# Kernel optimization log

Measured on AMD Instinct MI355X. Metric: run time of the kernel, lower is better.

## Reference

```python
import jax, jax.numpy as jnp
import numpy as np
from jax import lax

EPS = 1e-8
SLOPE = 0.2

def _modconv(x, wv, W, b, sW, sB, demodulate, pad):
    # StyleGAN2 modulated conv, expressed in the equivalent fused form:
    # scale input by per-sample style s, shared-weight conv, then demodulate output.
    s = wv @ sW.T + sB                                   # [B, Cin]
    y = lax.conv_general_dilated(
        x * s[:, :, None, None], W, (1, 1), [(pad, pad), (pad, pad)],
        dimension_numbers=("NCHW", "OIHW", "NCHW"))      # [B, Cout, H, W]
    if demodulate:
        # d[b,o] = 1/sqrt(sum_{i,k,k} (W[o,i,k,k]*s[b,i])^2 + eps)
        d = lax.rsqrt(jnp.einsum("oihw,bi->bo", W * W, s * s) + EPS)
        y = y * d[:, :, None, None]
    return y + b[None, :, None, None]

def _up2(x):
    B, C, H, W = x.shape
    # matches torch F.interpolate(scale_factor=2, mode='bilinear', align_corners=False)
    return jax.image.resize(x, (B, C, 2 * H, 2 * W), method="bilinear")

def setup_inputs() -> dict:
    B, CIN, COUT, NZ, H = 8, 512, 512, 512, 32
    key = jax.random.key(0)
    ks = jax.random.split(key, 20)
    wscale3 = 1.0 / np.sqrt(CIN * 9)   # kaiming-ish equalized-lr scale baked into weights
    wscale1 = 1.0 / np.sqrt(COUT)
    sscale = 1.0 / np.sqrt(NZ)
    return {
        "maps": jax.random.normal(ks[0], (B, CIN, H, H), jnp.float32),
        "w": jax.random.normal(ks[1], (B, NZ), jnp.float32),
        "rgb": jax.random.normal(ks[2], (B, 3, H, H), jnp.float32),
        "noise0": jax.random.normal(ks[3], (B, 1, 2 * H, 2 * H), jnp.float32),
        "noise1": jax.random.normal(ks[4], (B, 1, 2 * H, 2 * H), jnp.float32),
        "w0": jax.random.normal(ks[5], (COUT, CIN, 3, 3), jnp.float32) * wscale3,
        "b0": jnp.zeros((COUT,), jnp.float32),
        "sW0": jax.random.normal(ks[6], (CIN, NZ), jnp.float32) * sscale,
        "sB0": jnp.ones((CIN,), jnp.float32),
        "ns0": jax.random.normal(ks[7], (COUT,), jnp.float32) * 0.1,
        "w1": jax.random.normal(ks[8], (COUT, COUT, 3, 3), jnp.float32) * wscale3,
        "b1": jnp.zeros((COUT,), jnp.float32),
        "sW1": jax.random.normal(ks[9], (COUT, NZ), jnp.float32) * sscale,
        "sB1": jnp.ones((COUT,), jnp.float32),
        "ns1": jax.random.normal(ks[10], (COUT,), jnp.float32) * 0.1,
        "rgbW": jax.random.normal(ks[11], (3, COUT, 1, 1), jnp.float32) * wscale1,
        "rgbB": jnp.zeros((3,), jnp.float32),
        "rgbSW": jax.random.normal(ks[12], (COUT, NZ), jnp.float32) * sscale,
        "rgbSB": jnp.ones((COUT,), jnp.float32),
    }

def reference(maps, w, rgb, noise0, noise1,
              w0, b0, sW0, sB0, ns0,
              w1, b1, sW1, sB1, ns1,
              rgbW, rgbB, rgbSW, rgbSB):
    rgb = _up2(rgb)
    x = _up2(maps)
    # layer 0: modulated conv 3x3 + noise + leakyrelu
    x = _modconv(x, w, w0, b0, sW0, sB0, True, 1)
    x = x + ns0[None, :, None, None] * noise0
    x = jnp.where(x >= 0, x, SLOPE * x)
    # layer 1
    x = _modconv(x, w, w1, b1, sW1, sB1, True, 1)
    x = x + ns1[None, :, None, None] * noise1
    x = jnp.where(x >= 0, x, SLOPE * x)
    # to_rgb: modulated 1x1 conv, no demodulation
    rgb_out = rgb + _modconv(x, w, rgbW, rgbB, rgbSW, rgbSB, False, 0)
    return (rgb_out, x)
```

## Files before the change

kernel.cpp:

```cpp
#include <hip/hip_runtime.h>

typedef unsigned short u16;
typedef short bf16x8 __attribute__((ext_vector_type(8)));
typedef float f32x4 __attribute__((ext_vector_type(4)));
typedef u16 u16x4 __attribute__((ext_vector_type(4)));
typedef u16 u16x8 __attribute__((ext_vector_type(8)));
typedef unsigned u32x4 __attribute__((ext_vector_type(4)));

__device__ __forceinline__ float b2f(u16 v) {
  union { unsigned u; float f; } x; x.u = ((unsigned)v) << 16; return x.f;
}
__device__ __forceinline__ u16 f2b(float f) {
  unsigned u = __float_as_uint(f);
  unsigned r = (u + 0x7FFFu + ((u >> 16) & 1u)) >> 16;
  return (u16)r;
}
__device__ __forceinline__ float rin(const void* p, size_t i, int bf) {
  return bf ? b2f(((const u16*)p)[i]) : ((const float*)p)[i];
}
__device__ __forceinline__ void async16(const void* g, void* l) {
  __builtin_amdgcn_global_load_lds((const __attribute__((address_space(1))) unsigned*)g,
                                   (__attribute__((address_space(3))) unsigned*)l, 16, 0, 0);
}
__device__ __forceinline__ int detect_bf(const unsigned* __restrict__ w0raw, int tid, int* shflag) {
  if (tid < 64) {
    const unsigned lo = w0raw[tid] & 0xFFFFu;
    const unsigned e = (lo >> 7) & 0xFFu;
    const unsigned long long bad = __ballot(e < 100u || e > 126u);
    if (tid == 0) *shflag = (bad == 0ull) ? 1 : 0;
  }
  __syncthreads();
  return *shflag;
}

__global__ void styleall_kernel(const void* __restrict__ w,
                                const void* __restrict__ sW0, const void* __restrict__ sB0,
                                const void* __restrict__ sW1, const void* __restrict__ sB1,
                                const void* __restrict__ sWR, const void* __restrict__ sBR,
                                float* __restrict__ s0, float* __restrict__ s1,
                                float* __restrict__ sR, const unsigned* __restrict__ w0raw) {
  __shared__ int shflag;
  const int tid = threadIdx.x;
  const int bf = detect_bf(w0raw, tid, &shflag);
  const int mat = blockIdx.z, b = blockIdx.y, oc = blockIdx.x;
  const void* sW = (mat == 0) ? sW0 : ((mat == 1) ? sW1 : sWR);
  const void* sB = (mat == 0) ? sB0 : ((mat == 1) ? sB1 : sBR);
  float* out = (mat == 0) ? s0 : ((mat == 1) ? s1 : sR);
  const int i = oc * 64 + (tid >> 2), q = tid & 3;
  float acc = 0.f;
  if (bf) {
    const u16* rp = (const u16*)sW + (size_t)i * 512 + q * 128;
    const u16* wp = (const u16*)w + b * 512 + q * 128;
    for (int z = 0; z < 128; z += 8) {
      u16x8 a = *(const u16x8*)(rp + z), c = *(const u16x8*)(wp + z);
#pragma unroll
      for (int j = 0; j < 8; ++j) acc += b2f(a[j]) * b2f(c[j]);
    }
  } else {
    const float* rp = (const float*)sW + (size_t)i * 512 + q * 128;
    const float* wp = (const float*)w + b * 512 + q * 128;
    for (int z = 0; z < 128; z += 4) {
      f32x4 a = *(const f32x4*)(rp + z), c = *(const f32x4*)(wp + z);
#pragma unroll
      for (int j = 0; j < 4; ++j) acc += a[j] * c[j];
    }
  }
  acc += __shfl_xor(acc, 1, 64);
  acc += __shfl_xor(acc, 2, 64);
  if (q == 0) out[b * 512 + i] = acc + rin(sB, i, bf);
}

__global__ void demod_kernel(const void* __restrict__ W0, const void* __restrict__ W1,
                             const float* __restrict__ s0, const float* __restrict__ s1,
                             float* __restrict__ dm0, float* __restrict__ dm1,
                             u16* __restrict__ Wp0, u16* __restrict__ Wp1,
                             const unsigned* __restrict__ w0raw) {
  __shared__ int shflag;
  __shared__ float wl[4608];
  __shared__ float wsq[512];
  const int tid = threadIdx.x, lane = tid & 63, wv = tid >> 6;
  const int bf = detect_bf(w0raw, tid, &shflag);
  const int o = blockIdx.x, layer = blockIdx.y;
  const void* W = layer ? W1 : W0;
  const float* s = layer ? s1 : s0;
  float* d = layer ? dm1 : dm0;
  u16* Wp = layer ? Wp1 : Wp0;

  if (bf) {
    const u16* src = (const u16*)W + (size_t)o * 4608;
    for (int e = tid; e < 576; e += 256) {
      u16x8 v = *(const u16x8*)(src + e * 8);
#pragma unroll
      for (int j = 0; j < 8; ++j) wl[e * 8 + j] = b2f(v[j]);
    }
  } else {
    const float* src = (const float*)W + (size_t)o * 4608;
    for (int e = tid; e < 1152; e += 256) {
      f32x4 v = *(const f32x4*)(src + e * 4);
#pragma unroll
      for (int j = 0; j < 4; ++j) wl[e * 4 + j] = v[j];
    }
  }
  __syncthreads();
  for (int i = tid; i < 512; i += 256) {
    float ss = 0.f;
#pragma unroll
    for (int t = 0; t < 9; ++t) {
      const float f = wl[i * 9 + t];
      ss += f * f;
      Wp[t * 262144 + o * 512 + i] = f2b(f);
    }
    wsq[i] = ss;
  }
  __syncthreads();
#pragma unroll
  for (int bb = 0; bb < 2; ++bb) {
    const int b = wv * 2 + bb;
    float part = 0.f;
    for (int i = lane; i < 512; i += 64) { const float sv = s[b * 512 + i]; part += wsq[i] * sv * sv; }
#pragma unroll
    for (int st = 1; st < 64; st <<= 1) part += __shfl_xor(part, st, 64);
    if (lane == 0) d[b * 512 + o] = rsqrtf(part + 1e-8f);
  }
}

__global__ void prep_kernel(u16* __restrict__ actB, u32x4* __restrict__ zr, int NB) {
  const int id = blockIdx.x, tid = threadIdx.x;
  if (id < NB * 65) {
    const int bl = id / 65, sub = id - bl * 65;
    const int c = sub * 256 + tid;
    const int px = c >> 6, seg = c & 63;
    int oy, ox;
    if (px < 66)       { oy = 0;  ox = px; }
    else if (px < 132) { oy = 65; ox = px - 66; }
    else { const int e = px - 132; oy = 1 + (e >> 1); ox = (e & 1) * 65; }
    u32x4 z = {0, 0, 0, 0};
    *(u32x4*)&actB[((size_t)(bl * 4356) + oy * 66 + ox) * 512 + seg * 8] = z;
  } else {
    const int c = (id - NB * 65) * 256 + tid;
    if (c < 24832) { u32x4 z = {0, 0, 0, 0}; zr[c] = z; }
  }
}

__global__ void upsample_kernel(const void* __restrict__ maps, const float* __restrict__ s,
                                void* __restrict__ outb, int b_base,
                                const unsigned* __restrict__ w0raw) {
  __shared__ int shflag;
  __shared__ float it[32][2][33];
  const int tid = threadIdx.x;
  const int bf = detect_bf(w0raw, tid, &shflag);
  const size_t esz = bf ? 2 : 4;
  u16* xg = (u16*)((char*)outb + (98304 + (size_t)(b_base >> 2) * 8388608) * esz);
  int oy, i0, bl;
  if (gridDim.z == 8) {
    const int id = blockIdx.x + (blockIdx.y << 6) + (blockIdx.z << 10);
    bl = id & 7; const int r = id >> 3; oy = r & 63; i0 = (r >> 6) << 5;
  } else {
    oy = blockIdx.x; i0 = blockIdx.y << 5; bl = blockIdx.z;
  }
  const int bg = b_base + bl;
  const int m = oy >> 1;
  int iy0, iy1; float wy0, wy1;
  if ((oy & 1) == 0) { iy0 = (m > 0) ? m - 1 : 0; iy1 = m; wy0 = 0.25f; wy1 = 0.75f; }
  else               { iy0 = m; iy1 = (m < 31) ? m + 1 : 31; wy0 = 0.75f; wy1 = 0.25f; }
#pragma unroll
  for (int k = 0; k < 8; ++k) {
    const int e = tid + k * 256;
    const int c = e >> 6, wsel = (e >> 5) & 1, x = e & 31;
    const int iy = wsel ? iy1 : iy0;
    it[c][wsel][x] = rin(maps, ((size_t)(bg * 512 + i0 + c) * 32 + iy) * 32 + x, bf);
  }
  __syncthreads();
#pragma unroll
  for (int k = 0; k < 8; ++k) {
    const int e = tid + k * 256;
    const int xx = e >> 5, c = e & 31;
    const int mx = xx >> 1;
    int ix0, ix1; float wx0, wx1;
    if ((xx & 1) == 0) { ix0 = (mx > 0) ? mx - 1 : 0; ix1 = mx; wx0 = 0.25f; wx1 = 0.75f; }
    else               { ix0 = mx; ix1 = (mx < 31) ? mx + 1 : 31; wx0 = 0.75f; wx1 = 0.25f; }
    const float r0 = wx0 * it[c][0][ix0] + wx1 * it[c][0][ix1];
    const float r1 = wx0 * it[c][1][ix0] + wx1 * it[c][1][ix1];
    const float v = (wy0 * r0 + wy1 * r1) * s[bg * 512 + i0 + c];
    xg[((size_t)(bl * 4096) + oy * 64 + xx) * 512 + i0 + c] = f2b(v);
  }
}

template <int L>
__global__ __launch_bounds__(256, 2) void conv_kernel(
    void* __restrict__ outb, u16* __restrict__ actBp,
    const u16* __restrict__ Wp, const float* __restrict__ dmod,
    const void* __restrict__ bias, const void* __restrict__ nsc,
    const void* __restrict__ noise, const float* __restrict__ saux,
    const u16* __restrict__ zbuf, const void* __restrict__ rgbW,
    float* __restrict__ rgbacc, int b_base,
    const unsigned* __restrict__ w0raw) {
  __shared__ __attribute__((aligned(16))) u16 lds[32768];
  __shared__ float rgbWl[L == 1 ? 1536 : 4];
  __shared__ int shflag;
  const int tid = threadIdx.x, lane = tid & 63, w = tid >> 6;
  const int bf = detect_bf(w0raw, tid, &shflag);
  const size_t esz = bf ? 2 : 4;

  const int lin = blockIdx.x + (blockIdx.y << 5) + (blockIdx.z << 7);
  const int cpx = (int)(gridDim.z << 4);
  const int wg = (lin & 7) * cpx + (lin >> 3);
  const int bl = wg >> 7, rem = wg & 127;
  const int o0 = (rem >> 5) << 7, n0 = (rem & 31) << 7;
  const int bg = b_base + bl;
  const int wm = w >> 1, wn = w & 1;

  if constexpr (L == 1) {
    for (int e = tid; e < 1536; e += 256) rgbWl[e] = rin(rgbW, e, bf);
  }
  const u16* xg = (const u16*)((const char*)outb +
                  (98304 + (size_t)(b_base >> 2) * 8388608) * esz);

  const int q = lane >> 4, m15 = lane & 15;
  const int lro = m15 * 64 + ((q ^ (lane & 7)) * 8);
  const int srow8 = lane >> 3, schunk = (lane & 7) ^ srow8;
  const size_t aAst = (size_t)(o0 + srow8) * 512 + schunk * 8;

  const int sbase = (w & 1) * 2 + (w >> 1) * 8;
  int oyv[4], oxv[4];
  size_t pB[4];
  {
    const int kk4[4] = {sbase, sbase + 1, sbase + 4, sbase + 5};
#pragma unroll
    for (int j = 0; j < 4; ++j) {
      const int p = n0 + kk4[j] * 8 + srow8;
      const int oy = p >> 6, ox = p & 63;
      oyv[j] = oy; oxv[j] = ox;
      pB[j] = ((size_t)bl * 4356 + oy * 66 + ox) * 512 + schunk * 8;
    }
  }

  const u16* bBase[4];
  int koff, aoffu;
  auto setTap = [&](int tn_) {
    const int ty_ = (tn_ * 11) >> 5, tx_ = tn_ - ty_ * 3;
    koff = 0;
    aoffu = tn_ * 262144;
    if constexpr (L == 0) {
#pragma unroll
      for (int j = 0; j < 4; ++j) {
        const int iy_ = oyv[j] + ty_ - 1, ix_ = oxv[j] + tx_ - 1;
        bBase[j] = (((unsigned)iy_ < 64u) & ((unsigned)ix_ < 64u))
          ? (xg + ((size_t)((bl << 12) + (iy_ << 6) + ix_) * 512 + schunk * 8))
          : (zbuf + schunk * 8);
      }
    } else {
      const int sb_ = (ty_ * 66 + tx_) * 512;
#pragma unroll
      for (int j = 0; j < 4; ++j) bBase[j] = actBp + pB[j] + sb_;
    }
  };

#define STAGE_A(k_) \
  async16(Wp + aAst + (size_t)aoffu + (size_t)(k_) * 4096, &lds[stb + (k_) * 512])
#define STAGE_B(j_, k_) \
  async16(bBase[j_] + koff, &lds[stb + 8192 + (k_) * 512])

  f32x4 acc[4][4] = {};
  {
    setTap(0);
    const int stb = 0;
    STAGE_A(sbase); STAGE_A(sbase + 1);
    STAGE_A(sbase + 4); STAGE_A(sbase + 5);
    STAGE_B(0, sbase); STAGE_B(1, sbase + 1);
    STAGE_B(2, sbase + 4); STAGE_B(3, sbase + 5);
  }
  koff = 64; aoffu = 64;
  asm volatile("s_waitcnt vmcnt(0)" ::: "memory");
  __builtin_amdgcn_s_barrier();

  int arA  = wm * 4096 + lro;
  int arAx = wm * 4096 + (lro ^ 32);
  int arB  = 8192 + wn * 4096 + lro;
  int arBx = 8192 + wn * 4096 + (lro ^ 32);
  int stb  = 16384;

  bf16x8 afr[2][2], bfr[4][2];
#pragma unroll 1
  for (int s = 0; s < 72; ++s) {
    const int s1 = s + 1, ok = (s1 < 72);
    if (ok && (s1 & 7) == 0) setTap(s1 >> 3);

#pragma unroll
    for (int ni = 0; ni < 4; ++ni) {
      bfr[ni][0] = *(const bf16x8*)&lds[arB + ni * 1024];
      bfr[ni][1] = *(const bf16x8*)&lds[arBx + ni * 1024];
    }
#pragma unroll
    for (int mi = 0; mi < 2; ++mi) {
      afr[mi][0] = *(const bf16x8*)&lds[arA + mi * 1024];
      afr[mi][1] = *(const bf16x8*)&lds[arAx + mi * 1024];
    }
    if (ok) {
      STAGE_A(sbase); STAGE_A(sbase + 1);
      STAGE_B(0, sbase); STAGE_B(1, sbase + 1);
    }
    __builtin_amdgcn_s_setprio(1);
#pragma unroll
    for (int mi = 0; mi < 2; ++mi)
#pragma unroll
      for (int ni = 0; ni < 4; ++ni)
#pragma unroll
        for (int kk = 0; kk < 2; ++kk)
          acc[mi][ni] = __builtin_amdgcn_mfma_f32_16x16x32_bf16(
              afr[mi][kk], bfr[ni][kk], acc[mi][ni], 0, 0, 0);
    __builtin_amdgcn_s_setprio(0);
    if (ok) { asm volatile("s_waitcnt vmcnt(4)" ::: "memory"); }
    else    { asm volatile("s_waitcnt vmcnt(0)" ::: "memory"); }
    __builtin_amdgcn_s_barrier();

#pragma unroll
    for (int mi = 0; mi < 2; ++mi) {
      afr[mi][0] = *(const bf16x8*)&lds[arA + 2048 + mi * 1024];
      afr[mi][1] = *(const bf16x8*)&lds[arAx + 2048 + mi * 1024];
    }
    if (ok) {
      STAGE_B(2, sbase + 4); STAGE_B(3, sbase + 5);
      STAGE_A(sbase + 4); STAGE_A(sbase + 5);
    }
    __builtin_amdgcn_s_setprio(1);
#pragma unroll
    for (int mi = 0; mi < 2; ++mi)
#pragma unroll
      for (int ni = 0; ni < 4; ++ni)
#pragma unroll
        for (int kk = 0; kk < 2; ++kk)
          acc[2 + mi][ni] = __builtin_amdgcn_mfma_f32_16x16x32_bf16(
              afr[mi][kk], bfr[ni][kk], acc[2 + mi][ni], 0, 0, 0);
    __builtin_amdgcn_s_setprio(0);
    if (ok) { asm volatile("s_waitcnt vmcnt(2)" ::: "memory"); }
    __builtin_amdgcn_s_barrier();

    arA ^= 16384; arAx ^= 16384; arB ^= 16384; arBx ^= 16384; stb ^= 16384;
    koff += 64; aoffu += 64;
  }
#undef STAGE_A
#undef STAGE_B

  if constexpr (L == 0) {
#pragma unroll
    for (int ai = 0; ai < 4; ++ai) {
      const int o = o0 + wm * 64 + ai * 16 + q * 4;
      const f32x4 dv = *(const f32x4*)&dmod[bg * 512 + o];
      const f32x4 sv = *(const f32x4*)&saux[bg * 512 + o];
      float bv[4], nv[4];
#pragma unroll
      for (int r = 0; r < 4; ++r) { bv[r] = rin(bias, o + r, bf); nv[r] = rin(nsc, o + r, bf); }
#pragma unroll
      for (int bj = 0; bj < 4; ++bj) {
        const int p = n0 + wn * 64 + bj * 16 + m15;
        const float np = rin(noise, (size_t)bg * 4096 + p, bf);
        u16x4 pack;
#pragma unroll
        for (int r = 0; r < 4; ++r) {
          float v = acc[ai][bj][r] * dv[r] + bv[r] + nv[r] * np;
          v = (v >= 0.f) ? v : 0.2f * v;
          pack[r] = f2b(v * sv[r]);
        }
        const int oy = p >> 6, ox = p & 63;
        *(u16x4*)&actBp[((size_t)(bl * 4356) + (oy + 1) * 66 + (ox + 1)) * 512 + o] = pack;
      }
    }
  } else {
    char* xreg = (char*)outb + 98304 * esz;
    float racc[4][3] = {};
#pragma unroll
    for (int ai = 0; ai < 4; ++ai) {
      const int o = o0 + wm * 64 + ai * 16 + q * 4;
      const f32x4 dv = *(const f32x4*)&dmod[bg * 512 + o];
      const f32x4 srv = *(const f32x4*)&saux[bg * 512 + o];
      float bv[4], nv[4], w0l[4], w1l[4], w2l[4];
#pragma unroll
      for (int r = 0; r < 4; ++r) {
        bv[r] = rin(bias, o + r, bf); nv[r] = rin(nsc, o + r, bf);
        w0l[r] = rgbWl[o + r]; w1l[r] = rgbWl[512 + o + r]; w2l[r] = rgbWl[1024 + o + r];
      }
#pragma unroll
      for (int bj = 0; bj < 4; ++bj) {
        const int p = n0 + wn * 64 + bj * 16 + m15;
        const float np = rin(noise, (size_t)bg * 4096 + p, bf);
#pragma unroll
        for (int r = 0; r < 4; ++r) {
          float v = acc[ai][bj][r] * dv[r] + bv[r] + nv[r] * np;
          v = (v >= 0.f) ? v : 0.2f * v;
          const size_t xi = (size_t)(bg * 512 + o + r) * 4096 + p;
          if (bf) ((u16*)xreg)[xi] = f2b(v); else ((float*)xreg)[xi] = v;
          const float xr = v * srv[r];
          racc[bj][0] += w0l[r] * xr;
          racc[bj][1] += w1l[r] * xr;
          racc[bj][2] += w2l[r] * xr;
        }
      }
    }
#pragma unroll
    for (int bj = 0; bj < 4; ++bj) {
      const int p = n0 + wn * 64 + bj * 16 + m15;
#pragma unroll
      for (int c = 0; c < 3; ++c) {
        float t = racc[bj][c];
        t += __shfl_xor(t, 16, 64);
        t += __shfl_xor(t, 32, 64);
        if (lane < 16) atomicAdd(&rgbacc[(size_t)(bg * 3 + c) * 4096 + p], t);
      }
    }
  }
}

__global__ void rgbfin_kernel(const float* __restrict__ rgbacc, const void* __restrict__ rgbB,
                              const void* __restrict__ rgb, void* __restrict__ outb,
                              const unsigned* __restrict__ w0raw) {
  __shared__ int shflag;
  const int tid = threadIdx.x;
  const int bf = detect_bf(w0raw, tid, &shflag);
  const int g = blockIdx.x * 256 + tid;
  const int b = g >> 12, p = g & 4095;
  const int oy = p >> 6, ox = p & 63;
  const int m = oy >> 1; int iy0, iy1; float wy0, wy1;
  if ((oy & 1) == 0) { iy0 = (m > 0) ? m - 1 : 0; iy1 = m; wy0 = 0.25f; wy1 = 0.75f; }
  else               { iy0 = m; iy1 = (m < 31) ? m + 1 : 31; wy0 = 0.75f; wy1 = 0.25f; }
  const int mx = ox >> 1; int ix0, ix1; float wx0, wx1;
  if ((ox & 1) == 0) { ix0 = (mx > 0) ? mx - 1 : 0; ix1 = mx; wx0 = 0.25f; wx1 = 0.75f; }
  else               { ix0 = mx; ix1 = (mx < 31) ? mx + 1 : 31; wx0 = 0.75f; wx1 = 0.25f; }
#pragma unroll
  for (int c = 0; c < 3; ++c) {
    const size_t rb = (size_t)(b * 3 + c) * 1024;
    const float up = wy0 * (wx0 * rin(rgb, rb + iy0 * 32 + ix0, bf) + wx1 * rin(rgb, rb + iy0 * 32 + ix1, bf))
                   + wy1 * (wx0 * rin(rgb, rb + iy1 * 32 + ix0, bf) + wx1 * rin(rgb, rb + iy1 * 32 + ix1, bf));
    const float v = up + rin(rgbB, c, bf) + rgbacc[(size_t)(b * 3 + c) * 4096 + p];
    const size_t oi = ((size_t)(b * 3 + c) << 12) + p;
    if (bf) ((u16*)outb)[oi] = f2b(v); else ((float*)outb)[oi] = v;
  }
}


extern "C" void kernel_launch(void* const* d_in, const int* in_sizes, int n_in,
                              void* d_out, int out_size, void* d_ws, size_t ws_size,
                              hipStream_t stream) {
  const void* maps   = d_in[0];
  const void* wlat   = d_in[1];
  const void* rgb    = d_in[2];
  const void* noise0 = d_in[3];
  const void* noise1 = d_in[4];
  const void* w0     = d_in[5];
  const void* b0     = d_in[6];
  const void* sW0    = d_in[7];
  const void* sB0    = d_in[8];
  const void* ns0    = d_in[9];
  const void* w1     = d_in[10];
  const void* b1     = d_in[11];
  const void* sW1    = d_in[12];
  const void* sB1    = d_in[13];
  const void* ns1    = d_in[14];
  const void* rgbW   = d_in[15];
  const void* rgbB   = d_in[16];
  const void* rgbSW  = d_in[17];
  const void* rgbSB  = d_in[18];
  const unsigned* w0raw = (const unsigned*)w0;

  char* ws = (char*)d_ws;
  float* s0     = (float*)(ws + 1024);
  float* s1     = (float*)(ws + 17408);
  float* sR     = (float*)(ws + 33792);
  float* dm0    = (float*)(ws + 50176);
  float* dm1    = (float*)(ws + 66560);
  u16*   zbuf   = (u16*)(ws + 82944);
  float* rgbacc = (float*)(ws + 87040);
  u16*   Wp0    = (u16*)(ws + 480256);
  u16*   Wp1    = (u16*)(ws + 5198848);
  u16*   actB   = (u16*)(ws + 9917440);

  const bool full = ws_size >= (size_t)(9917440 + 35684352);
  const int NB = full ? 8 : 4;

  styleall_kernel<<<dim3(8, 8, 3), 256, 0, stream>>>(wlat, sW0, sB0, sW1, sB1, rgbSW, rgbSB,
                                                     s0, s1, sR, w0raw);
  demod_kernel<<<dim3(512, 2), 256, 0, stream>>>(w0, w1, s0, s1, dm0, dm1, Wp0, Wp1, w0raw);
  prep_kernel<<<NB * 65 + 97, 256, 0, stream>>>(actB, (u32x4*)zbuf, NB);

  for (int pass = 0; pass < 8 / NB; ++pass) {
    const int b_base = pass * NB;
    upsample_kernel<<<dim3(64, 16, NB), 256, 0, stream>>>(maps, s0, d_out, b_base, w0raw);
    conv_kernel<0><<<dim3(32, 4, NB), 256, 0, stream>>>(d_out, actB, Wp0, dm0,
        b0, ns0, noise0, s1, zbuf, nullptr, nullptr, b_base, w0raw);
    conv_kernel<1><<<dim3(32, 4, NB), 256, 0, stream>>>(d_out, actB, Wp1, dm1,
        b1, ns1, noise1, sR, zbuf, rgbW, rgbacc, b_base, w0raw);
  }
  rgbfin_kernel<<<128, 256, 0, stream>>>(rgbacc, rgbB, rgb, d_out, w0raw);
}
```

Baseline: 512.6 us.

## Enlarge conv tile to 128x256 with 512 threads and triple-buffered K=32 pipeline

Reorganizes the implicit-GEMM conv kernel into 512-thread workgroups covering 128 output channels by 256 pixels. The K step changes from 64 to 32 with a three-stage LDS ring buffer, replacing the double-buffered two-half schedule. Each warp now stages its own A and B slices and runs one barrier per step. This aims to raise operand reuse per LDS load and deepen load prefetch, at the cost of more LDS per block, more barriers overall, and register pressure under the stricter launch bounds.

```diff
diff --git a/kernel.cpp b/kernel.cpp
--- a/kernel.cpp
+++ b/kernel.cpp
@@ -187,7 +187,7 @@
 }
 
 template <int L>
-__global__ __launch_bounds__(256, 2) void conv_kernel(
+__global__ __launch_bounds__(512, 4) void conv_kernel(
     void* __restrict__ outb, u16* __restrict__ actBp,
     const u16* __restrict__ Wp, const float* __restrict__ dmod,
     const void* __restrict__ bias, const void* __restrict__ nsc,
@@ -195,47 +195,43 @@
     const u16* __restrict__ zbuf, const void* __restrict__ rgbW,
     float* __restrict__ rgbacc, int b_base,
     const unsigned* __restrict__ w0raw) {
-  __shared__ __attribute__((aligned(16))) u16 lds[32768];
+  __shared__ __attribute__((aligned(16))) u16 lds[36864];
   __shared__ float rgbWl[L == 1 ? 1536 : 4];
   __shared__ int shflag;
   const int tid = threadIdx.x, lane = tid & 63, w = tid >> 6;
   const int bf = detect_bf(w0raw, tid, &shflag);
   const size_t esz = bf ? 2 : 4;
 
-  const int lin = blockIdx.x + (blockIdx.y << 5) + (blockIdx.z << 7);
-  const int cpx = (int)(gridDim.z << 4);
+  const int lin = blockIdx.x + (blockIdx.y << 4) + (blockIdx.z << 6);
+  const int cpx = (int)(gridDim.z << 3);
   const int wg = (lin & 7) * cpx + (lin >> 3);
-  const int bl = wg >> 7, rem = wg & 127;
-  const int o0 = (rem >> 5) << 7, n0 = (rem & 31) << 7;
+  const int bl = wg >> 6, rem = wg & 63;
+  const int o0 = (rem >> 4) << 7, n0 = (rem & 15) << 8;
   const int bg = b_base + bl;
-  const int wm = w >> 1, wn = w & 1;
+  const int wm = w >> 2, wn = w & 3;
 
   if constexpr (L == 1) {
-    for (int e = tid; e < 1536; e += 256) rgbWl[e] = rin(rgbW, e, bf);
+    for (int e = tid; e < 1536; e += 512) rgbWl[e] = rin(rgbW, e, bf);
   }
   const u16* xg = (const u16*)((const char*)outb +
                   (98304 + (size_t)(b_base >> 2) * 8388608) * esz);
 
   const int q = lane >> 4, m15 = lane & 15;
-  const int lro = m15 * 64 + ((q ^ (lane & 7)) * 8);
-  const int srow8 = lane >> 3, schunk = (lane & 7) ^ srow8;
-  const size_t aAst = (size_t)(o0 + srow8) * 512 + schunk * 8;
-
-  const int sbase = (w & 1) * 2 + (w >> 1) * 8;
-  int oyv[4], oxv[4];
-  size_t pB[4];
-  {
-    const int kk4[4] = {sbase, sbase + 1, sbase + 4, sbase + 5};
-#pragma unroll
-    for (int j = 0; j < 4; ++j) {
-      const int p = n0 + kk4[j] * 8 + srow8;
-      const int oy = p >> 6, ox = p & 63;
-      oyv[j] = oy; oxv[j] = ox;
-      pB[j] = ((size_t)bl * 4356 + oy * 66 + ox) * 512 + schunk * 8;
-    }
-  }
-
-  const u16* bBase[4];
+  const int laneAB = m15 * 32 + ((q ^ (m15 & 3)) * 8);
+  const int sr = lane >> 2;
+  const int lcs = (lane & 3) ^ (sr & 3);
+  const u16* aSrc = Wp + (size_t)(o0 + w * 16 + sr) * 512 + lcs * 8;
+
+  int oyv[2], oxv[2];
+  size_t pB[2];
+#pragma unroll
+  for (int j = 0; j < 2; ++j) {
+    const int p = n0 + w * 32 + j * 16 + sr;
+    oyv[j] = p >> 6; oxv[j] = p & 63;
+    pB[j] = ((size_t)bl * 4356 + oyv[j] * 66 + oxv[j]) * 512 + lcs * 8;
+  }
+
+  const u16* bBase[2];
   int koff, aoffu;
   auto setTap = [&](int tn_) {
     const int ty_ = (tn_ * 11) >> 5, tx_ = tn_ - ty_ * 3;
@@ -243,101 +239,66 @@
     aoffu = tn_ * 262144;
     if constexpr (L == 0) {
 #pragma unroll
-      for (int j = 0; j < 4; ++j) {
+      for (int j = 0; j < 2; ++j) {
         const int iy_ = oyv[j] + ty_ - 1, ix_ = oxv[j] + tx_ - 1;
         bBase[j] = (((unsigned)iy_ < 64u) & ((unsigned)ix_ < 64u))
-          ? (xg + ((size_t)((bl << 12) + (iy_ << 6) + ix_) * 512 + schunk * 8))
-          : (zbuf + schunk * 8);
+          ? (xg + ((size_t)((bl << 12) + (iy_ << 6) + ix_) * 512 + lcs * 8))
+          : (zbuf + lcs * 8);
       }
     } else {
       const int sb_ = (ty_ * 66 + tx_) * 512;
 #pragma unroll
-      for (int j = 0; j < 4; ++j) bBase[j] = actBp + pB[j] + sb_;
+      for (int j = 0; j < 2; ++j) bBase[j] = actBp + pB[j] + sb_;
     }
   };
 
-#define STAGE_A(k_) \
-  async16(Wp + aAst + (size_t)aoffu + (size_t)(k_) * 4096, &lds[stb + (k_) * 512])
-#define STAGE_B(j_, k_) \
-  async16(bBase[j_] + koff, &lds[stb + 8192 + (k_) * 512])
+#define STAGE_A() async16(aSrc + aoffu + koff, &lds[sto + w * 512])
+#define STAGE_B(j_) async16(bBase[j_] + koff, &lds[sto + 4096 + w * 1024 + (j_) * 512])
 
   f32x4 acc[4][4] = {};
+  int rdo = 0, sto = 0;
   {
     setTap(0);
-    const int stb = 0;
-    STAGE_A(sbase); STAGE_A(sbase + 1);
-    STAGE_A(sbase + 4); STAGE_A(sbase + 5);
-    STAGE_B(0, sbase); STAGE_B(1, sbase + 1);
-    STAGE_B(2, sbase + 4); STAGE_B(3, sbase + 5);
-  }
-  koff = 64; aoffu = 64;
+    STAGE_A(); STAGE_B(0); STAGE_B(1);
+    sto = 12288; koff = 32;
+    STAGE_A(); STAGE_B(0); STAGE_B(1);
+    sto = 24576; koff = 64;
+  }
   asm volatile("s_waitcnt vmcnt(0)" ::: "memory");
   __builtin_amdgcn_s_barrier();
 
-  int arA  = wm * 4096 + lro;
-  int arAx = wm * 4096 + (lro ^ 32);
-  int arB  = 8192 + wn * 4096 + lro;
-  int arBx = 8192 + wn * 4096 + (lro ^ 32);
-  int stb  = 16384;
-
-  bf16x8 afr[2][2], bfr[4][2];
+  bf16x8 afr[4], bfr[4];
 #pragma unroll 1
-  for (int s = 0; s < 72; ++s) {
-    const int s1 = s + 1, ok = (s1 < 72);
-    if (ok && (s1 & 7) == 0) setTap(s1 >> 3);
-
-#pragma unroll
-    for (int ni = 0; ni < 4; ++ni) {
-      bfr[ni][0] = *(const bf16x8*)&lds[arB + ni * 1024];
-      bfr[ni][1] = *(const bf16x8*)&lds[arBx + ni * 1024];
-    }
-#pragma unroll
-    for (int mi = 0; mi < 2; ++mi) {
-      afr[mi][0] = *(const bf16x8*)&lds[arA + mi * 1024];
-      afr[mi][1] = *(const bf16x8*)&lds[arAx + mi * 1024];
-    }
-    if (ok) {
-      STAGE_A(sbase); STAGE_A(sbase + 1);
-      STAGE_B(0, sbase); STAGE_B(1, sbase + 1);
-    }
+  for (int s = 0; s < 144; ++s) {
+    const int s2 = s + 2, ok2 = (s2 < 144);
+    if (ok2 && (s2 & 15) == 0) setTap(s2 >> 4);
+
+#pragma unroll
+    for (int ni = 0; ni < 4; ++ni)
+      bfr[ni] = *(const bf16x8*)&lds[rdo + 4096 + wn * 2048 + ni * 512 + laneAB];
+#pragma unroll
+    for (int mi = 0; mi < 4; ++mi)
+      afr[mi] = *(const bf16x8*)&lds[rdo + wm * 2048 + mi * 512 + laneAB];
+
+    if (ok2) { STAGE_A(); STAGE_B(0); STAGE_B(1); }
+
     __builtin_amdgcn_s_setprio(1);
 #pragma unroll
-    for (int mi = 0; mi < 2; ++mi)
+    for (int mi = 0; mi < 4; ++mi)
 #pragma unroll
       for (int ni = 0; ni < 4; ++ni)
-#pragma unroll
-        for (int kk = 0; kk < 2; ++kk)
-          acc[mi][ni] = __builtin_amdgcn_mfma_f32_16x16x32_bf16(
-              afr[mi][kk], bfr[ni][kk], acc[mi][ni], 0, 0, 0);
+        acc[mi][ni] = __builtin_amdgcn_mfma_f32_16x16x32_bf16(
+            afr[mi], bfr[ni], acc[mi][ni], 0, 0, 0);
     __builtin_amdgcn_s_setprio(0);
-    if (ok) { asm volatile("s_waitcnt vmcnt(4)" ::: "memory"); }
-    else    { asm volatile("s_waitcnt vmcnt(0)" ::: "memory"); }
-    __builtin_amdgcn_s_barrier();
-
-#pragma unroll
-    for (int mi = 0; mi < 2; ++mi) {
-      afr[mi][0] = *(const bf16x8*)&lds[arA + 2048 + mi * 1024];
-      afr[mi][1] = *(const bf16x8*)&lds[arAx + 2048 + mi * 1024];
-    }
-    if (ok) {
-      STAGE_B(2, sbase + 4); STAGE_B(3, sbase + 5);
-      STAGE_A(sbase + 4); STAGE_A(sbase + 5);
-    }
-    __builtin_amdgcn_s_setprio(1);
-#pragma unroll
-    for (int mi = 0; mi < 2; ++mi)
-#pragma unroll
-      for (int ni = 0; ni < 4; ++ni)
-#pragma unroll
-        for (int kk = 0; kk < 2; ++kk)
-          acc[2 + mi][ni] = __builtin_amdgcn_mfma_f32_16x16x32_bf16(
-              afr[mi][kk], bfr[ni][kk], acc[2 + mi][ni], 0, 0, 0);
-    __builtin_amdgcn_s_setprio(0);
-    if (ok) { asm volatile("s_waitcnt vmcnt(2)" ::: "memory"); }
-    __builtin_amdgcn_s_barrier();
-
-    arA ^= 16384; arAx ^= 16384; arB ^= 16384; arBx ^= 16384; stb ^= 16384;
-    koff += 64; aoffu += 64;
+
+    if (s < 143) {
+      if (ok2) { asm volatile("s_waitcnt vmcnt(3)" ::: "memory"); }
+      else     { asm volatile("s_waitcnt vmcnt(0)" ::: "memory"); }
+      __builtin_amdgcn_s_barrier();
+    }
+    rdo = (rdo == 24576) ? 0 : rdo + 12288;
+    sto = (sto == 24576) ? 0 : sto + 12288;
+    koff += 32;
   }
 #undef STAGE_A
 #undef STAGE_B
@@ -485,9 +446,9 @@
   for (int pass = 0; pass < 8 / NB; ++pass) {
     const int b_base = pass * NB;
     upsample_kernel<<<dim3(64, 16, NB), 256, 0, stream>>>(maps, s0, d_out, b_base, w0raw);
-    conv_kernel<0><<<dim3(32, 4, NB), 256, 0, stream>>>(d_out, actB, Wp0, dm0,
+    conv_kernel<0><<<dim3(16, 4, NB), 512, 0, stream>>>(d_out, actB, Wp0, dm0,
         b0, ns0, noise0, s1, zbuf, nullptr, nullptr, b_base, w0raw);
-    conv_kernel<1><<<dim3(32, 4, NB), 256, 0, stream>>>(d_out, actB, Wp1, dm1,
+    conv_kernel<1><<<dim3(16, 4, NB), 512, 0, stream>>>(d_out, actB, Wp1, dm1,
         b1, ns1, noise1, sR, zbuf, rgbW, rgbacc, b_base, w0raw);
   }
   rgbfin_kernel<<<128, 256, 0, stream>>>(rgbacc, rgbB, rgb, d_out, w0raw);
```

New measurement: 481.8 us. 1.06x faster.
